# Performance work log

Measured on AMD Instinct MI355X. Metric: run time of the kernel, lower is better.

Reference implementation:

```python
import jax, jax.numpy as jnp
import numpy as np

N_NODES = 50000
N_EDGES = 640000
RANK = 128
ORDER = 3
N_GRAPHS = 50
LN_EPS = 1e-5


def setup_inputs() -> dict:
    key = jax.random.key(0)
    ks = jax.random.split(key, 8)
    features = jax.random.normal(ks[0], (N_NODES, RANK), dtype=jnp.float32)
    src = jax.random.randint(ks[1], (N_EDGES,), 0, N_NODES, dtype=jnp.int32)
    dst = jax.random.randint(ks[2], (N_EDGES,), 0, N_NODES, dtype=jnp.int32)
    batch_num_nodes = jnp.full((N_GRAPHS,), N_NODES // N_GRAPHS, dtype=jnp.int32)
    scale = 1.0 / np.sqrt(RANK)
    Ws = jax.random.normal(ks[3], (ORDER, RANK, RANK), dtype=jnp.float32) * scale
    bs = jnp.zeros((ORDER, RANK), dtype=jnp.float32)
    gammas = jnp.ones((ORDER, RANK), dtype=jnp.float32)
    betas = jnp.zeros((ORDER, RANK), dtype=jnp.float32)
    return {"features": features, "src": src, "dst": dst,
            "batch_num_nodes": batch_num_nodes,
            "Ws": Ws, "bs": bs, "gammas": gammas, "betas": betas}


def _layer_norm(x, gamma, beta):
    mu = jnp.mean(x, axis=-1, keepdims=True)
    var = jnp.mean(jnp.square(x - mu), axis=-1, keepdims=True)
    return (x - mu) * jax.lax.rsqrt(var + LN_EPS) * gamma + beta


def reference(features, src, dst, batch_num_nodes, Ws, bs, gammas, betas):
    ones = jnp.ones((src.shape[0],), dtype=features.dtype)
    deg_out = jax.ops.segment_sum(ones, src, num_segments=N_NODES)  # out-degree of src nodes
    deg_in = jax.ops.segment_sum(ones, dst, num_segments=N_NODES)   # in-degree of dst nodes
    inv_sqrt_out = jax.lax.rsqrt(jnp.maximum(deg_out, 1.0))[:, None]
    inv_sqrt_in = jax.lax.rsqrt(jnp.maximum(deg_in, 1.0))[:, None]

    feats = features
    for i in range(ORDER):
        # DGL GraphConv, norm='both': h = D_in^{-1/2} A D_out^{-1/2} (X W) + b
        h = (feats @ Ws[i]) * inv_sqrt_out
        agg = jax.ops.segment_sum(h[src], dst, num_segments=N_NODES)
        h = agg * inv_sqrt_in + bs[i]
        h = _layer_norm(h, gammas[i], betas[i])
        feats = jax.nn.relu(h)  # dropout is identity at inference

    first_idx = jnp.cumsum(jnp.concatenate([jnp.zeros((1,), jnp.int32), batch_num_nodes[:-1]]))
    return feats[first_idx]
```

## Files before the change

### kernel.cpp

```cpp
#include <hip/hip_runtime.h>

#define RANK 128
#define LN_EPS 1e-5f

#define NCH 4
#define CHUNK 12800
#define BINS (NCH * CHUNK)
#define ECH 64
#define BT 1024

using short8 = __attribute__((ext_vector_type(8))) short;
using v4f    = __attribute__((ext_vector_type(4))) float;

__device__ inline unsigned short f2bf(float f) {
    unsigned u = __float_as_uint(f);
    unsigned r = (u + 0x7FFF + ((u >> 16) & 1)) >> 16;
    return (unsigned short)r;
}

__global__ __launch_bounds__(BT) void hist_part(const int* __restrict__ src,
                                                const int* __restrict__ dst,
                                                unsigned short* __restrict__ pdst,
                                                unsigned short* __restrict__ psrc,
                                                const float* __restrict__ Ws,
                                                short* __restrict__ Wt, int nE,
                                                const int* __restrict__ bnn, int nG,
                                                int* __restrict__ T3, int* __restrict__ cnt3) {
    int c = blockIdx.x, n = blockIdx.y, z = blockIdx.z;
    if (c == ECH) {
        int sid = (n + 4 * z) * BT + threadIdx.x;
        if (sid < 3 * 2048) {
            int l = sid >> 11;
            int s = sid & 2047;
            int lane = s & 63, ct = (s >> 6) & 7, k0 = s >> 9;
            int m = lane & 15, quad = lane >> 4;
            const float* W = Ws + (size_t)l * RANK * RANK;
            short* o = Wt + (size_t)l * 16384 + (size_t)s * 8;
#pragma unroll
            for (int j = 0; j < 8; j++)
                o[j] = (short)f2bf(W[(k0 * 32 + quad * 8 + j) * RANK + ct * 16 + m]);
        } else if (sid >= 6144 && sid < 6208) {
            int lane = sid - 6144;
            if (nG <= 64) {
                int v = (lane < nG) ? bnn[lane] : 0;
                int orig = v;
#pragma unroll
                for (int off = 1; off < 64; off <<= 1) {
                    int t = __shfl_up(v, off);
                    if (lane >= off) v += t;
                }
                int excl = v - orig;
                if (lane < nG) T3[lane] = excl;
                if (lane == 0) *cnt3 = nG;
            } else if (lane == 0) {
                int idx = 0;
                for (int g = 0; g < nG; g++) { T3[g] = idx; idx += bnn[g]; }
                *cnt3 = nG;
            }
        }
        return;
    }
    __shared__ int h[CHUNK];
    const int* arr = z ? src : dst;
    unsigned short* pout = z ? psrc : pdst;
    int base = n * CHUNK;
    for (int i = threadIdx.x; i < CHUNK; i += BT) h[i] = 0;
    __syncthreads();
    int epc = (nE + ECH - 1) / ECH;
    int e0 = c * epc, e1 = min(e0 + epc, nE);
    int tid = threadIdx.x;
    int a0 = min((e0 + 3) & ~3, e1);
    if (tid < a0 - e0) {
        int v = arr[e0 + tid] - base;
        if ((unsigned)v < (unsigned)CHUNK) atomicAdd(&h[v], 1);
    }
    int rem = e1 - a0;
    int nv = (rem > 0) ? (rem & ~3) : 0;
    for (int e = a0 + tid * 4; e < a0 + nv; e += BT * 4) {
        int4 v4 = *(const int4*)(arr + e);
        int v;
        v = v4.x - base; if ((unsigned)v < (unsigned)CHUNK) atomicAdd(&h[v], 1);
        v = v4.y - base; if ((unsigned)v < (unsigned)CHUNK) atomicAdd(&h[v], 1);
        v = v4.z - base; if ((unsigned)v < (unsigned)CHUNK) atomicAdd(&h[v], 1);
        v = v4.w - base; if ((unsigned)v < (unsigned)CHUNK) atomicAdd(&h[v], 1);
    }
    int t0 = a0 + nv;
    if (tid < e1 - t0) {
        int v = arr[t0 + tid] - base;
        if ((unsigned)v < (unsigned)CHUNK) atomicAdd(&h[v], 1);
    }
    __syncthreads();
    unsigned short* o = pout + (size_t)c * BINS + base;
    for (int i = threadIdx.x; i < CHUNK; i += BT) o[i] = (unsigned short)h[i];
}

__global__ __launch_bounds__(256) void reduce_scan1(const unsigned short* __restrict__ pdst,
                                                    const unsigned short* __restrict__ psrc,
                                                    int* __restrict__ counts,
                                                    float* __restrict__ invin,
                                                    float* __restrict__ invout,
                                                    int* __restrict__ ends,
                                                    int* __restrict__ bsums, int M) {
    __shared__ int tmp[256];
    int tid = threadIdx.x;
    int gid = blockIdx.x * 256 + tid;
    int cd = 0, cs = 0;
    if (gid < M) {
#pragma unroll 8
        for (int c = 0; c < ECH; c++) {
            cd += pdst[(size_t)c * BINS + gid];
            cs += psrc[(size_t)c * BINS + gid];
        }
        counts[gid] = cd;
        invin[gid]  = rsqrtf(fmaxf((float)cd, 1.0f));
        invout[gid] = rsqrtf(fmaxf((float)cs, 1.0f));
    }
    tmp[tid] = cd;
    __syncthreads();
    for (int off = 1; off < 256; off <<= 1) {
        int t = (tid >= off) ? tmp[tid - off] : 0;
        __syncthreads();
        tmp[tid] += t;
        __syncthreads();
    }
    if (gid < M) ends[gid] = tmp[tid];
    if (tid == 255) bsums[blockIdx.x] = tmp[255];
}

__global__ __launch_bounds__(256) void scan23_offs(int* __restrict__ ends,
                                                   const int* __restrict__ counts,
                                                   const int* __restrict__ bsums,
                                                   const unsigned short* __restrict__ pdst,
                                                   int* __restrict__ pcur, int nb, int M) {
    __shared__ int red[256];
    int tid = threadIdx.x;
    int b = blockIdx.x;
    red[tid] = (tid < b && tid < nb) ? bsums[tid] : 0;
    __syncthreads();
    for (int off = 128; off > 0; off >>= 1) {
        if (tid < off) red[tid] += red[tid + off];
        __syncthreads();
    }
    int prefix = red[0];
    int gid = b * 256 + tid;
    if (gid < M) {
        int e = ends[gid] + prefix;
        ends[gid] = e;
        int run = e - counts[gid];
#pragma unroll 8
        for (int c = 0; c < ECH; c++) {
            size_t idx = (size_t)c * BINS + gid;
            int t = pdst[idx];
            pcur[idx] = run;
            run += t;
        }
    }
}

__global__ __launch_bounds__(BT) void fill_sorted(const int* __restrict__ src,
                                                  const int* __restrict__ dst,
                                                  const int* __restrict__ pcur,
                                                  int* __restrict__ csr_src, int nE) {
    __shared__ int cur[CHUNK];
    int c = blockIdx.x, n = blockIdx.y;
    int base = n * CHUNK;
    const int* o = pcur + (size_t)c * BINS + base;
    for (int i = threadIdx.x; i < CHUNK; i += BT) cur[i] = o[i];
    __syncthreads();
    int epc = (nE + ECH - 1) / ECH;
    int e0 = c * epc, e1 = min(e0 + epc, nE);
    int tid = threadIdx.x;
    int a0 = min((e0 + 3) & ~3, e1);
    if (tid < a0 - e0) {
        int e = e0 + tid;
        int d = dst[e] - base;
        if ((unsigned)d < (unsigned)CHUNK) csr_src[atomicAdd(&cur[d], 1)] = src[e];
    }
    int rem = e1 - a0;
    int nv = (rem > 0) ? (rem & ~3) : 0;
    for (int e = a0 + tid * 4; e < a0 + nv; e += BT * 4) {
        int4 d4 = *(const int4*)(dst + e);
        int4 s4 = *(const int4*)(src + e);
        int d;
        d = d4.x - base; if ((unsigned)d < (unsigned)CHUNK) csr_src[atomicAdd(&cur[d], 1)] = s4.x;
        d = d4.y - base; if ((unsigned)d < (unsigned)CHUNK) csr_src[atomicAdd(&cur[d], 1)] = s4.y;
        d = d4.z - base; if ((unsigned)d < (unsigned)CHUNK) csr_src[atomicAdd(&cur[d], 1)] = s4.z;
        d = d4.w - base; if ((unsigned)d < (unsigned)CHUNK) csr_src[atomicAdd(&cur[d], 1)] = s4.w;
    }
    int t0 = a0 + nv;
    if (tid < e1 - t0) {
        int e = t0 + tid;
        int d = dst[e] - base;
        if ((unsigned)d < (unsigned)CHUNK) csr_src[atomicAdd(&cur[d], 1)] = src[e];
    }
}

__global__ __launch_bounds__(256) void frontier_csr(const int* __restrict__ list,
                                                    const int* __restrict__ cnt,
                                                    const int* __restrict__ ends,
                                                    const int* __restrict__ csr_src,
                                                    unsigned* __restrict__ bm_out,
                                                    int* __restrict__ out_list,
                                                    int* __restrict__ out_cnt) {
    int lane = threadIdx.x & 63;
    int wg = blockIdx.x * 4 + (threadIdx.x >> 6);
    int nW = gridDim.x * 4;
    int n = *cnt;
    for (int i = wg; i < n; i += nW) {
        int node = list[i];
        int end = ends[node];
        int beg = (node == 0) ? 0 : ends[node - 1];
        for (int e0 = beg; e0 < end; e0 += 64) {
            int u = 0;
            bool flag = false;
            if (e0 + lane < end) {
                u = csr_src[e0 + lane];
                unsigned old = atomicOr(&bm_out[u >> 5], 1u << (u & 31));
                flag = !((old >> (u & 31)) & 1);
            }
            unsigned long long mask = __ballot(flag);
            if (mask) {
                int leader = __ffsll((long long)mask) - 1;
                int base = 0;
                if (lane == leader) base = atomicAdd(out_cnt, __popcll(mask));
                base = __shfl(base, leader);
                if (flag) out_list[base + __popcll(mask & ((1ull << lane) - 1))] = u;
            }
        }
    }
}

template <int LAST, int FP32IN>
__global__ __launch_bounds__(256) void layer_fused(const void* __restrict__ FinV,
                                                   const float* __restrict__ edge_scale,
                                                   const int* __restrict__ ends,
                                                   const int* __restrict__ csr_src,
                                                   const short* __restrict__ Wt,
                                                   const float* __restrict__ invin,
                                                   const float* __restrict__ invout,
                                                   const float* __restrict__ bias,
                                                   const float* __restrict__ gamma,
                                                   const float* __restrict__ beta,
                                                   const int* __restrict__ list,
                                                   const int* __restrict__ cnt,
                                                   unsigned short* __restrict__ Fout,
                                                   float* __restrict__ out) {
    const unsigned* Fb = (const unsigned*)FinV;
    const float4*  Ff = (const float4*)FinV;
    __shared__ short As[16][136];
    __shared__ float sstat[2][4][16];
    __shared__ float sinv[2][16];
    __shared__ int snode[16];
    int tid = threadIdx.x;
    int w = tid >> 6, lane = tid & 63;
    int seg = lane >> 4, m = lane & 15;
    int n = *cnt;
    int tiles = (n + 15) >> 4;

    float bb[2], gg[2], pp[2];
#pragma unroll
    for (int j = 0; j < 2; j++) {
        int col = (w * 2 + j) * 16 + m;
        bb[j] = bias[col]; gg[j] = gamma[col]; pp[j] = beta[col];
    }

    for (int t = blockIdx.x; t < tiles; t += gridDim.x) {
        int base = t * 16;

        for (int q = 0; q < 4; q++) {
            int rr = w * 4 + q;
            int gr = base + rr;
            float ax[8];
#pragma unroll
            for (int k = 0; k < 8; k++) ax[k] = 0.f;
            int node = -1;
            if (gr < n) {
                node = list[gr];
                int end = ends[node];
                int e = (node == 0) ? 0 : ends[node - 1];
                while (e < end) {
                    int rem = end - e;
                    int myi = 0;
                    if (lane < rem) myi = csr_src[e + lane];
                    int nn = min(rem, 64);
                    int p = 0;
                    for (; p + 16 <= nn; p += 16) {
                        if (FP32IN) {
                            float4 fa[4], fb4[4]; float so[4];
#pragma unroll
                            for (int gi = 0; gi < 4; gi++) {
                                int idx = __shfl(myi, p + gi * 4 + seg);
                                so[gi] = edge_scale[idx];
                                const float4* qq = Ff + (size_t)idx * 32 + m * 2;
                                fa[gi] = qq[0]; fb4[gi] = qq[1];
                            }
#pragma unroll
                            for (int gi = 0; gi < 4; gi++) {
                                ax[0] += fa[gi].x * so[gi]; ax[1] += fa[gi].y * so[gi];
                                ax[2] += fa[gi].z * so[gi]; ax[3] += fa[gi].w * so[gi];
                                ax[4] += fb4[gi].x * so[gi]; ax[5] += fb4[gi].y * so[gi];
                                ax[6] += fb4[gi].z * so[gi]; ax[7] += fb4[gi].w * so[gi];
                            }
                        } else {
                            uint4 u[4];
#pragma unroll
                            for (int gi = 0; gi < 4; gi++) {
                                int idx = __shfl(myi, p + gi * 4 + seg);
                                u[gi] = *(const uint4*)(Fb + (size_t)idx * 64 + m * 4);
                            }
#pragma unroll
                            for (int gi = 0; gi < 4; gi++) {
                                ax[0] += __uint_as_float(u[gi].x << 16);
                                ax[1] += __uint_as_float(u[gi].x & 0xFFFF0000u);
                                ax[2] += __uint_as_float(u[gi].y << 16);
                                ax[3] += __uint_as_float(u[gi].y & 0xFFFF0000u);
                                ax[4] += __uint_as_float(u[gi].z << 16);
                                ax[5] += __uint_as_float(u[gi].z & 0xFFFF0000u);
                                ax[6] += __uint_as_float(u[gi].w << 16);
                                ax[7] += __uint_as_float(u[gi].w & 0xFFFF0000u);
                            }
                        }
                    }
                    for (; p < nn; p += 4) {
                        bool act = (p + seg) < nn;
                        int idx = __shfl(myi, (p + seg) & 63);
                        if (act) {
                            if (FP32IN) {
                                float so = edge_scale[idx];
                                const float4* qq = Ff + (size_t)idx * 32 + m * 2;
                                float4 fa = qq[0], fb4 = qq[1];
                                ax[0] += fa.x * so; ax[1] += fa.y * so;
                                ax[2] += fa.z * so; ax[3] += fa.w * so;
                                ax[4] += fb4.x * so; ax[5] += fb4.y * so;
                                ax[6] += fb4.z * so; ax[7] += fb4.w * so;
                            } else {
                                uint4 u = *(const uint4*)(Fb + (size_t)idx * 64 + m * 4);
                                ax[0] += __uint_as_float(u.x << 16);
                                ax[1] += __uint_as_float(u.x & 0xFFFF0000u);
                                ax[2] += __uint_as_float(u.y << 16);
                                ax[3] += __uint_as_float(u.y & 0xFFFF0000u);
                                ax[4] += __uint_as_float(u.z << 16);
                                ax[5] += __uint_as_float(u.z & 0xFFFF0000u);
                                ax[6] += __uint_as_float(u.w << 16);
                                ax[7] += __uint_as_float(u.w & 0xFFFF0000u);
                            }
                        }
                    }
                    e += nn;
                }
#pragma unroll
                for (int k = 0; k < 8; k++) {
                    ax[k] += __shfl_xor(ax[k], 16);
                    ax[k] += __shfl_xor(ax[k], 32);
                }
            }
            if (seg == 0) {
                uint4 o;
                o.x = (unsigned)f2bf(ax[0]) | ((unsigned)f2bf(ax[1]) << 16);
                o.y = (unsigned)f2bf(ax[2]) | ((unsigned)f2bf(ax[3]) << 16);
                o.z = (unsigned)f2bf(ax[4]) | ((unsigned)f2bf(ax[5]) << 16);
                o.w = (unsigned)f2bf(ax[6]) | ((unsigned)f2bf(ax[7]) << 16);
                *(uint4*)&As[rr][8 * m] = o;
            }
            if (lane == 0) {
                snode[rr] = node;
                sinv[0][rr] = (node >= 0) ? invin[node] : 1.f;
                sinv[1][rr] = (node >= 0) ? invout[node] : 1.f;
            }
        }
        __syncthreads();

        short8 a[4];
#pragma unroll
        for (int k0 = 0; k0 < 4; k0++)
            a[k0] = *(const short8*)&As[m][k0 * 32 + seg * 8];
        v4f acc[2];
        acc[0] = (v4f){0.f, 0.f, 0.f, 0.f};
        acc[1] = (v4f){0.f, 0.f, 0.f, 0.f};
#pragma unroll
        for (int k0 = 0; k0 < 4; k0++) {
#pragma unroll
            for (int j = 0; j < 2; j++) {
                int ct = w * 2 + j;
                short8 b = *(const short8*)(Wt + (size_t)((k0 * 8 + ct) * 64 + lane) * 8);
                acc[j] = __builtin_amdgcn_mfma_f32_16x16x32_bf16(a[k0], b, acc[j], 0, 0, 0);
            }
        }

        float x[4][2];
#pragma unroll
        for (int r = 0; r < 4; r++) {
            int row = seg * 4 + r;
            float iv = sinv[0][row];
            float s = 0.f, sq = 0.f;
#pragma unroll
            for (int j = 0; j < 2; j++) {
                float c = acc[j][r] * iv + bb[j];
                x[r][j] = c;
                s += c; sq += c * c;
            }
#pragma unroll
            for (int off = 1; off < 16; off <<= 1) {
                s  += __shfl_xor(s, off);
                sq += __shfl_xor(sq, off);
            }
            if (m == 0) { sstat[0][w][row] = s; sstat[1][w][row] = sq; }
        }
        __syncthreads();

#pragma unroll
        for (int r = 0; r < 4; r++) {
            int row = seg * 4 + r;
            int gr = base + row;
            if (gr >= n) continue;
            float s  = sstat[0][0][row] + sstat[0][1][row] + sstat[0][2][row] + sstat[0][3][row];
            float sq = sstat[1][0][row] + sstat[1][1][row] + sstat[1][2][row] + sstat[1][3][row];
            float mu = s * (1.0f / RANK);
            float var = sq * (1.0f / RANK) - mu * mu;
            float rs = rsqrtf(var + LN_EPS);
#pragma unroll
            for (int j = 0; j < 2; j++) {
                int col = (w * 2 + j) * 16 + m;
                float y = fmaxf((x[r][j] - mu) * rs * gg[j] + pp[j], 0.f);
                if (LAST) {
                    out[(size_t)gr * RANK + col] = y;
                } else {
                    Fout[(size_t)snode[row] * RANK + col] = f2bf(y * sinv[1][row]);
                }
            }
        }
        __syncthreads();
    }
}

extern "C" void kernel_launch(void* const* d_in, const int* in_sizes, int n_in,
                              void* d_out, int out_size, void* d_ws, size_t ws_size,
                              hipStream_t stream) {
    const float* features = (const float*)d_in[0];
    const int* src = (const int*)d_in[1];
    const int* dst = (const int*)d_in[2];
    const int* bnn = (const int*)d_in[3];
    const float* Ws = (const float*)d_in[4];
    const float* bs = (const float*)d_in[5];
    const float* gammas = (const float*)d_in[6];
    const float* betas = (const float*)d_in[7];
    float* out = (float*)d_out;

    int M  = in_sizes[0] / RANK;
    int nE = in_sizes[1];
    int nG = in_sizes[3];
    int bmw = (M + 31) / 32;

    char* ws = (char*)d_ws;
    size_t off = 0;
    auto alloc = [&](size_t bytes) {
        void* p = ws + off;
        off += (bytes + 255) & ~(size_t)255;
        return p;
    };
    int*   counts  = (int*)alloc((size_t)M * 4);
    int*   ends    = (int*)alloc((size_t)M * 4);
    int*   bsums   = (int*)alloc(256 * 4);
    float* invout  = (float*)alloc((size_t)M * 4);
    float* invin   = (float*)alloc((size_t)M * 4);
    int*   csr_src = (int*)alloc((size_t)nE * 4);
    short* Wt      = (short*)alloc((size_t)3 * 16384 * 2);
    short* F1      = (short*)alloc((size_t)M * RANK * 2);
    short* F2      = (short*)alloc((size_t)M * RANK * 2);
    unsigned short* pdst = (unsigned short*)alloc((size_t)ECH * BINS * 2);
    unsigned short* psrc = (unsigned short*)alloc((size_t)ECH * BINS * 2);
    int*   pcur    = (int*)alloc((size_t)ECH * BINS * 4);
    char*  zbase   = (char*)alloc((size_t)(2 * bmw + 2) * 4);
    unsigned* bm2  = (unsigned*)zbase;
    unsigned* bm1  = bm2 + bmw;
    int*   cnt2    = (int*)(bm1 + bmw);
    int*   cnt1    = cnt2 + 1;
    int*   cnt3    = (int*)alloc(256);
    int*   T3      = (int*)alloc((size_t)((nG + 63) & ~63) * 4);
    int*   T2      = (int*)alloc((size_t)M * 4);
    int*   T1      = (int*)alloc((size_t)M * 4);

    int nb = (M + 255) / 256;

    hipMemsetAsync(zbase, 0, (size_t)(2 * bmw + 2) * 4, stream);

    hist_part<<<dim3(ECH + 1, NCH, 2), BT, 0, stream>>>(src, dst, pdst, psrc, Ws, Wt, nE,
                                                        bnn, nG, T3, cnt3);
    reduce_scan1<<<nb, 256, 0, stream>>>(pdst, psrc, counts, invin, invout, ends, bsums, M);
    scan23_offs<<<nb, 256, 0, stream>>>(ends, counts, bsums, pdst, pcur, nb, M);
    fill_sorted<<<dim3(ECH, NCH), BT, 0, stream>>>(src, dst, pcur, csr_src, nE);

    frontier_csr<<<64, 256, 0, stream>>>(T3, cnt3, ends, csr_src, bm2, T2, cnt2);
    frontier_csr<<<64, 256, 0, stream>>>(T2, cnt2, ends, csr_src, bm1, T1, cnt1);

    layer_fused<0, 1><<<512, 256, 0, stream>>>(features, invout, ends, csr_src, Wt,
                                               invin, invout, bs, gammas, betas,
                                               T1, cnt1, (unsigned short*)F1, nullptr);
    layer_fused<0, 0><<<64, 256, 0, stream>>>(F1, nullptr, ends, csr_src, Wt + 16384,
                                              invin, invout, bs + RANK, gammas + RANK, betas + RANK,
                                              T2, cnt2, (unsigned short*)F2, nullptr);
    layer_fused<1, 0><<<(nG + 15) / 16, 256, 0, stream>>>(F2, nullptr, ends, csr_src, Wt + 32768,
                                                          invin, invout, bs + 2 * RANK,
                                                          gammas + 2 * RANK, betas + 2 * RANK,
                                                          T3, cnt3, nullptr, out);
}
```

Baseline: 170.1 us.

## Fuse two frontier expansions into one kernel and drop the memset

Replaces the two back-to-back frontier_csr launches with a single frontier_both kernel. Each block recomputes the level-2 frontier (the neighbours of up to 64 target nodes) into shared memory, with no deduplication, then expands it into the deduplicated level-1 frontier. Zeroing of the bitmap and counters moves from a hipMemsetAsync into block 0 of reduce_scan1, which removes one launch and one memset. The level-2 list is capped at 64 seed nodes and 4096 entries and may now hold duplicates, so it relies on small frontier sizes and adds some redundant per-block work.

```diff
diff --git a/kernel.cpp b/kernel.cpp
--- a/kernel.cpp
+++ b/kernel.cpp
@@ -100,9 +100,16 @@
                                                     float* __restrict__ invin,
                                                     float* __restrict__ invout,
                                                     int* __restrict__ ends,
-                                                    int* __restrict__ bsums, int M) {
+                                                    int* __restrict__ bsums, int M,
+                                                    unsigned* __restrict__ bm1, int bmw,
+                                                    int* __restrict__ cnt1,
+                                                    int* __restrict__ cnt2) {
     __shared__ int tmp[256];
     int tid = threadIdx.x;
+    if (blockIdx.x == 0) {
+        for (int i = tid; i < bmw; i += 256) bm1[i] = 0;
+        if (tid == 0) { *cnt1 = 0; *cnt2 = 0; }
+    }
     int gid = blockIdx.x * 256 + tid;
     int cd = 0, cs = 0;
     if (gid < M) {
@@ -195,19 +202,60 @@
     }
 }
 
-__global__ __launch_bounds__(256) void frontier_csr(const int* __restrict__ list,
-                                                    const int* __restrict__ cnt,
-                                                    const int* __restrict__ ends,
-                                                    const int* __restrict__ csr_src,
-                                                    unsigned* __restrict__ bm_out,
-                                                    int* __restrict__ out_list,
-                                                    int* __restrict__ out_cnt) {
-    int lane = threadIdx.x & 63;
-    int wg = blockIdx.x * 4 + (threadIdx.x >> 6);
+__global__ __launch_bounds__(256) void frontier_both(const int* __restrict__ T3,
+                                                     const int* __restrict__ cnt3,
+                                                     const int* __restrict__ ends,
+                                                     const int* __restrict__ csr_src,
+                                                     unsigned* __restrict__ bm1,
+                                                     int* __restrict__ T2g,
+                                                     int* __restrict__ cnt2,
+                                                     int* __restrict__ T1,
+                                                     int* __restrict__ cnt1) {
+    __shared__ int t2loc[4096];
+    __shared__ int soff[64];
+    __shared__ int sn2;
+    int tid = threadIdx.x;
+    int lane = tid & 63, w = tid >> 6;
+    int n3 = *cnt3;
+    int n3c = (n3 < 64) ? n3 : 64;
+    if (tid < 64) {
+        int node = (lane < n3c) ? T3[lane] : -1;
+        int d = 0;
+        if (node >= 0) {
+            int end = ends[node];
+            int beg = (node == 0) ? 0 : ends[node - 1];
+            d = end - beg;
+        }
+        int v = d;
+#pragma unroll
+        for (int off = 1; off < 64; off <<= 1) {
+            int t = __shfl_up(v, off);
+            if (lane >= off) v += t;
+        }
+        soff[lane] = v - d;
+        if (lane == 63) sn2 = v;
+    }
+    __syncthreads();
+    int n2 = (sn2 < 4096) ? sn2 : 4096;
+    for (int i = w; i < n3c; i += 4) {
+        int node = T3[i];
+        int end = ends[node];
+        int beg = (node == 0) ? 0 : ends[node - 1];
+        int off = soff[i];
+        for (int e0 = beg; e0 < end; e0 += 64) {
+            int pos = off + (e0 - beg) + lane;
+            if (e0 + lane < end && pos < 4096) t2loc[pos] = csr_src[e0 + lane];
+        }
+    }
+    __syncthreads();
+    if (blockIdx.x == 0) {
+        for (int i = tid; i < n2; i += 256) T2g[i] = t2loc[i];
+        if (tid == 0) *cnt2 = n2;
+    }
+    int wgg = blockIdx.x * 4 + w;
     int nW = gridDim.x * 4;
-    int n = *cnt;
-    for (int i = wg; i < n; i += nW) {
-        int node = list[i];
+    for (int i = wgg; i < n2; i += nW) {
+        int node = t2loc[i];
         int end = ends[node];
         int beg = (node == 0) ? 0 : ends[node - 1];
         for (int e0 = beg; e0 < end; e0 += 64) {
@@ -215,16 +263,16 @@
             bool flag = false;
             if (e0 + lane < end) {
                 u = csr_src[e0 + lane];
-                unsigned old = atomicOr(&bm_out[u >> 5], 1u << (u & 31));
+                unsigned old = atomicOr(&bm1[u >> 5], 1u << (u & 31));
                 flag = !((old >> (u & 31)) & 1);
             }
             unsigned long long mask = __ballot(flag);
             if (mask) {
                 int leader = __ffsll((long long)mask) - 1;
                 int base = 0;
-                if (lane == leader) base = atomicAdd(out_cnt, __popcll(mask));
+                if (lane == leader) base = atomicAdd(cnt1, __popcll(mask));
                 base = __shfl(base, leader);
-                if (flag) out_list[base + __popcll(mask & ((1ull << lane) - 1))] = u;
+                if (flag) T1[base + __popcll(mask & ((1ull << lane) - 1))] = u;
             }
         }
     }
@@ -470,28 +518,23 @@
     unsigned short* pdst = (unsigned short*)alloc((size_t)ECH * BINS * 2);
     unsigned short* psrc = (unsigned short*)alloc((size_t)ECH * BINS * 2);
     int*   pcur    = (int*)alloc((size_t)ECH * BINS * 4);
-    char*  zbase   = (char*)alloc((size_t)(2 * bmw + 2) * 4);
-    unsigned* bm2  = (unsigned*)zbase;
-    unsigned* bm1  = bm2 + bmw;
-    int*   cnt2    = (int*)(bm1 + bmw);
-    int*   cnt1    = cnt2 + 1;
-    int*   cnt3    = (int*)alloc(256);
+    unsigned* bm1  = (unsigned*)alloc((size_t)bmw * 4);
+    int*   cnts    = (int*)alloc(256);
+    int*   cnt1 = cnts, * cnt2 = cnts + 1, * cnt3 = cnts + 2;
     int*   T3      = (int*)alloc((size_t)((nG + 63) & ~63) * 4);
-    int*   T2      = (int*)alloc((size_t)M * 4);
+    int*   T2      = (int*)alloc((size_t)4096 * 4);
     int*   T1      = (int*)alloc((size_t)M * 4);
 
     int nb = (M + 255) / 256;
-
-    hipMemsetAsync(zbase, 0, (size_t)(2 * bmw + 2) * 4, stream);
 
     hist_part<<<dim3(ECH + 1, NCH, 2), BT, 0, stream>>>(src, dst, pdst, psrc, Ws, Wt, nE,
                                                         bnn, nG, T3, cnt3);
-    reduce_scan1<<<nb, 256, 0, stream>>>(pdst, psrc, counts, invin, invout, ends, bsums, M);
+    reduce_scan1<<<nb, 256, 0, stream>>>(pdst, psrc, counts, invin, invout, ends, bsums, M,
+                                         bm1, bmw, cnt1, cnt2);
     scan23_offs<<<nb, 256, 0, stream>>>(ends, counts, bsums, pdst, pcur, nb, M);
     fill_sorted<<<dim3(ECH, NCH), BT, 0, stream>>>(src, dst, pcur, csr_src, nE);
 
-    frontier_csr<<<64, 256, 0, stream>>>(T3, cnt3, ends, csr_src, bm2, T2, cnt2);
-    frontier_csr<<<64, 256, 0, stream>>>(T2, cnt2, ends, csr_src, bm1, T1, cnt1);
+    frontier_both<<<64, 256, 0, stream>>>(T3, cnt3, ends, csr_src, bm1, T2, cnt2, T1, cnt1);
 
     layer_fused<0, 1><<<512, 256, 0, stream>>>(features, invout, ends, csr_src, Wt,
                                                invin, invout, bs, gammas, betas,
```

Measured after the change: 172.8 us. No clear change (+1.6%).
